# Performance work log

Hardware: AMD Instinct MI355X
Metric: run time of the kernel (lower is better)

## Reference

```python
import jax, jax.numpy as jnp
import numpy as np

B, S, D, H = 2, 2048, 1024, 16
HD = D // H  # head dim 64
LN_EPS = 1e-12


def setup_inputs() -> dict:
    key = jax.random.key(0)
    ks = jax.random.split(key, 10)
    sc = 0.02
    return {
        "input_tensor": jax.random.normal(ks[0], (B, S, D), dtype=jnp.float32),
        "attention_mask": jnp.zeros((B, 1, 1, S), dtype=jnp.float32),
        "Wq": jax.random.normal(ks[1], (D, D), dtype=jnp.float32) * sc,
        "bq": jnp.zeros((D,), dtype=jnp.float32),
        "Wk": jax.random.normal(ks[2], (D, D), dtype=jnp.float32) * sc,
        "bk": jnp.zeros((D,), dtype=jnp.float32),
        "Wv": jax.random.normal(ks[3], (D, D), dtype=jnp.float32) * sc,
        "bv": jnp.zeros((D,), dtype=jnp.float32),
        "Wo": jax.random.normal(ks[4], (D, D), dtype=jnp.float32) * sc,
        "bo": jnp.zeros((D,), dtype=jnp.float32),
        "ln_gamma": jnp.ones((D,), dtype=jnp.float32),
        "ln_beta": jnp.zeros((D,), dtype=jnp.float32),
    }


def _split_heads(x):
    # [B,S,D] -> [B,H,S,hd]
    return x.reshape(B, S, H, HD).transpose(0, 2, 1, 3)


def reference(input_tensor, attention_mask, Wq, bq, Wk, bk, Wv, bv, Wo, bo, ln_gamma, ln_beta):
    q = _split_heads(input_tensor @ Wq + bq)
    k = _split_heads(input_tensor @ Wk + bk)
    v = _split_heads(input_tensor @ Wv + bv)
    scores = jnp.einsum("bhqd,bhkd->bhqk", q, k) / jnp.sqrt(jnp.float32(HD))
    scores = scores + attention_mask  # additive mask broadcast
    probs = jax.nn.softmax(scores, axis=-1)
    ctx = jnp.einsum("bhqk,bhkd->bhqd", probs, v)
    ctx = ctx.transpose(0, 2, 1, 3).reshape(B, S, D)
    hidden = ctx @ Wo + bo
    x = hidden + input_tensor
    mu = jnp.mean(x, axis=-1, keepdims=True)
    var = jnp.mean(jnp.square(x - mu), axis=-1, keepdims=True)
    return (x - mu) / jnp.sqrt(var + LN_EPS) * ln_gamma + ln_beta
```

## Files before the change

### kernel.cpp

```cpp
#include <hip/hip_runtime.h>
#include <stdint.h>

#define Bb 2
#define Ss 2048
#define Dd 1024
#define Hh 16
#define HD 64
#define Mtot 4096

typedef __bf16 bf16x8 __attribute__((ext_vector_type(8)));
typedef float f32x4 __attribute__((ext_vector_type(4)));
typedef unsigned short ushort_t;

#if __has_builtin(__builtin_amdgcn_exp2f)
#define EXP2(x) __builtin_amdgcn_exp2f(x)
#else
#define EXP2(x) __expf((x) * 0.6931472f)
#endif

__device__ __forceinline__ float bf2f(ushort_t u) {
    union { uint32_t i; float f; } v;
    v.i = ((uint32_t)u) << 16;
    return v.f;
}

__device__ __forceinline__ ushort_t f2bf(float f) {
    union { float f; uint32_t i; } v;
    v.f = f;
    uint32_t u = v.i;
    u += 0x7FFFu + ((u >> 16) & 1u);
    return (ushort_t)(u >> 16);
}

__device__ __forceinline__ uint32_t fbits(float f) {
    union { float f; uint32_t i; } v; v.f = f; return v.i;
}

__device__ __forceinline__ float load_in(const void* p, size_t i, int isf32) {
    if (isf32) return ((const float*)p)[i];
    return bf2f(((const ushort_t*)p)[i]);
}

__device__ __forceinline__ void gload_lds16(const void* g, void* l) {
    __builtin_amdgcn_global_load_lds(
        (const __attribute__((address_space(1))) void*)g,
        (__attribute__((address_space(3))) void*)l, 16, 0, 0);
}

#define NCONV 4204544ull
__global__ __launch_bounds__(256) void prep_k(
    const void* X, const void* mask, const void* bq, const void* bk,
    const void* bv, const void* bo, const void* g, const void* be,
    const void* Wq, const void* Wk, const void* Wv, const void* Wo,
    int* __restrict__ flag, ushort_t* __restrict__ cX,
    ushort_t* __restrict__ cMask, ushort_t* __restrict__ cB,
    ushort_t* __restrict__ wt) {
    __shared__ int sflag;
    __shared__ ushort_t tile[32][33];
    const int tid = threadIdx.x;
    {
        const int lane = tid & 63;
        if (tid < 64) {
            const ushort_t* Xu = (const ushort_t*)X;
            int local = 0;
            for (int i = lane; i < 2048; i += 64) {
                int e = (Xu[i] >> 7) & 0xFF;
                local += (e >= 0x90);
            }
            for (int off = 1; off < 64; off <<= 1) local += __shfl_xor(local, off);
            if (lane == 0) sflag = (local >= 4) ? 1 : 0;
        }
    }
    __syncthreads();
    const int f = sflag;
    if (blockIdx.x == 0 && tid == 0) *flag = f;

    if (blockIdx.x < 1024) {
        const size_t stride = 1024ull * 256ull;
        for (size_t i = (size_t)blockIdx.x * 256 + tid; i < NCONV; i += stride) {
            if (i < 4194304ull) {
                cX[i] = f2bf(load_in(X, i, f));
            } else if (i < 4198400ull) {
                size_t j = i - 4194304ull;
                cMask[j] = f2bf(load_in(mask, j, f));
            } else {
                size_t j = i - 4198400ull;
                int w = (int)(j >> 10);
                size_t r = j & 1023ull;
                const void* p = (w == 0) ? bq : (w == 1) ? bk : (w == 2) ? bv
                              : (w == 3) ? bo : (w == 4) ? g : be;
                cB[w * 1024 + r] = f2bf(load_in(p, r, f));
            }
        }
    } else {
        int id2 = blockIdx.x - 1024;
        int z = id2 >> 10;
        int rem = id2 & 1023;
        int bx = rem & 31, by = rem >> 5;
        const void* W = (z == 0) ? Wq : (z == 1) ? Wk : (z == 2) ? Wv : Wo;
        ushort_t* T = wt + (size_t)z * Dd * Dd;
        int tx = tid & 31, ty = tid >> 5;
        int x = bx * 32 + tx;
        int y0 = by * 32;
        for (int i = 0; i < 4; i++) {
            int y = y0 + ty + i * 8;
            tile[ty + i * 8][tx] = f2bf(load_in(W, (size_t)y * Dd + x, f));
        }
        __syncthreads();
        int x2 = by * 32 + tx;
        int y20 = bx * 32;
        for (int i = 0; i < 4; i++) {
            int y = y20 + ty + i * 8;
            T[(size_t)y * Dd + x2] = tile[tx][ty + i * 8];
        }
    }
}

__global__ __launch_bounds__(256) void gemm_qkv(
    const ushort_t* __restrict__ X, const ushort_t* __restrict__ wt,
    const ushort_t* __restrict__ cB,
    ushort_t* __restrict__ Qb, ushort_t* __restrict__ Kb, ushort_t* __restrict__ Vtb) {
    const int z = blockIdx.z;
    const ushort_t* Wt = wt + (size_t)z * Dd * Dd;
    const ushort_t* bias = cB + z * 1024;

    __shared__ __align__(16) ushort_t smem[128 * 32 * 2];
    ushort_t* As = smem;
    ushort_t* Bs = smem + 128 * 32;

    const int tid = threadIdx.x;
    const int lane = tid & 63, wv = tid >> 6;
    const int quad = lane >> 4, l15 = lane & 15;
    const int wrow = (wv >> 1) * 64, wcol = (wv & 1) * 64;
    const int row0 = blockIdx.y * 128, col0 = blockIdx.x * 128;
    const int lrow = lane >> 2, lcol = (lane & 3) * 8;

    const f32x4 fzero = {0.f, 0.f, 0.f, 0.f};
    f32x4 acc[4][4];
    for (int mt = 0; mt < 4; mt++)
        for (int nt = 0; nt < 4; nt++) acc[mt][nt] = fzero;

    for (int k0 = 0; k0 < Dd; k0 += 32) {
        __syncthreads();
        for (int j = 0; j < 2; j++) {
            int ch = wv * 2 + j;
            gload_lds16(&X[(size_t)(row0 + ch * 16 + lrow) * Dd + k0 + lcol],
                        &As[ch * 512]);
            gload_lds16(&Wt[(size_t)(col0 + ch * 16 + lrow) * Dd + k0 + lcol],
                        &Bs[ch * 512]);
        }
        __syncthreads();
        bf16x8 af[4], bfr[4];
        for (int mt = 0; mt < 4; mt++)
            af[mt] = *(const bf16x8*)(&As[(wrow + mt * 16 + l15) * 32 + quad * 8]);
        for (int nt = 0; nt < 4; nt++)
            bfr[nt] = *(const bf16x8*)(&Bs[(wcol + nt * 16 + l15) * 32 + quad * 8]);
        for (int mt = 0; mt < 4; mt++)
            for (int nt = 0; nt < 4; nt++)
                acc[mt][nt] = __builtin_amdgcn_mfma_f32_16x16x32_bf16(
                    af[mt], bfr[nt], acc[mt][nt], 0, 0, 0);
    }

    const float qscale = 0.18033688f;
    ushort_t* Cs = smem;
    for (int mt = 0; mt < 4; mt++) {
        __syncthreads();
        for (int nt = 0; nt < 4; nt++) {
            int gn = col0 + wcol + nt * 16 + l15;
            float bv_ = bf2f(bias[gn]);
            for (int r = 0; r < 4; r++) {
                float v = acc[mt][nt][r] + bv_;
                if (z == 0) v *= qscale;
                int ric = (wv >> 1) * 16 + quad * 4 + r;
                Cs[ric * 136 + wcol + nt * 16 + l15] = f2bf(v);
            }
        }
        __syncthreads();
        if (z == 2) {
            int c = tid >> 1, r0 = (tid & 1) * 16;
            int gn = col0 + c, h = gn >> 6, d = gn & 63;
            int gmbase = row0 + (r0 >> 4) * 64 + mt * 16;
            int b = gmbase >> 11, s0 = gmbase & 2047;
            union { ushort_t u[16]; uint4 q[2]; } pk;
            for (int i = 0; i < 16; i++) pk.u[i] = Cs[(r0 + i) * 136 + c];
            uint4* dst = (uint4*)&Vtb[((size_t)((b * Hh + h) * HD + d)) * Ss + s0];
            dst[0] = pk.q[0];
            dst[1] = pk.q[1];
        } else {
            int ric = tid >> 3, c0 = (tid & 7) * 16;
            int gm = row0 + (ric >> 4) * 64 + mt * 16 + (ric & 15);
            int gn = col0 + c0, h = gn >> 6, d0 = gn & 63;
            int b = gm >> 11, s = gm & 2047;
            const uint4* src = (const uint4*)&Cs[ric * 136 + c0];
            ushort_t* Ob = (z == 0) ? Qb : Kb;
            uint4* dst = (uint4*)&Ob[((size_t)((b * Hh + h) * Ss + s)) * HD + d0];
            dst[0] = src[0];
            dst[1] = src[1];
        }
    }
}

#define STR 76
__global__ __launch_bounds__(512) void attn(
    const ushort_t* __restrict__ Q, const ushort_t* __restrict__ K,
    const ushort_t* __restrict__ Vt, const ushort_t* __restrict__ mask,
    ushort_t* __restrict__ ctx) {
    const int tid = threadIdx.x;
    const int lane = tid & 63, wv = tid >> 6;
    const int quad = lane >> 4, l15 = lane & 15;
    const int bh = blockIdx.x;
    const int b = bh >> 4, h = bh & 15;
    const int q0 = blockIdx.y * 128 + wv * 16;

    const ushort_t* Qh = Q + (size_t)bh * Ss * HD;
    const ushort_t* Kh = K + (size_t)bh * Ss * HD;
    const ushort_t* Vh = Vt + (size_t)bh * HD * Ss;

    __shared__ __align__(16) ushort_t Ks[2][64 * 64];
    __shared__ __align__(16) ushort_t Vs[2][64 * 64];
    __shared__ __align__(16) float maskF[Ss];
    __shared__ __align__(16) ushort_t Pl[8][16 * STR];
    ushort_t* Pw = &Pl[wv][0];

    for (int i = tid; i < Ss; i += 512)
        maskF[i] = (bf2f(mask[b * Ss + i]) - 4.0f) * 1.4426950f;

    const int r8 = lane >> 3, c8 = lane & 7, gc = c8 ^ r8;
    const int sw = l15 & 7;

    gload_lds16(&Kh[(size_t)(wv * 8 + r8) * HD + gc * 8], &Ks[0][wv * 512]);
    gload_lds16(&Vh[(size_t)(wv * 8 + r8) * Ss + gc * 8], &Vs[0][wv * 512]);

    bf16x8 qf[2];
    qf[0] = *(const bf16x8*)(&Qh[(size_t)(q0 + l15) * HD + quad * 8]);
    qf[1] = *(const bf16x8*)(&Qh[(size_t)(q0 + l15) * HD + 32 + quad * 8]);

    const f32x4 fzero = {0.f, 0.f, 0.f, 0.f};
    f32x4 o[4];
    for (int dt = 0; dt < 4; dt++) o[dt] = fzero;
    float l_part = 0.f;

    for (int kb = 0; kb < Ss; kb += 64) {
        const int buf = (kb >> 6) & 1;
        __syncthreads();

        if (kb + 64 < Ss) {
            gload_lds16(&Kh[(size_t)(kb + 64 + wv * 8 + r8) * HD + gc * 8],
                        &Ks[buf ^ 1][wv * 512]);
            gload_lds16(&Vh[(size_t)(wv * 8 + r8) * Ss + kb + 64 + gc * 8],
                        &Vs[buf ^ 1][wv * 512]);
        }

        const ushort_t* ks = &Ks[buf][0];
        const ushort_t* vs = &Vs[buf][0];

        f32x4 st[4];
        for (int kt = 0; kt < 4; kt++) {
            bf16x8 kf0 = *(const bf16x8*)(&ks[(kt * 16 + l15) * 64 + ((quad) ^ sw) * 8]);
            bf16x8 kf1 = *(const bf16x8*)(&ks[(kt * 16 + l15) * 64 + ((quad + 4) ^ sw) * 8]);
            st[kt] = __builtin_amdgcn_mfma_f32_16x16x32_bf16(kf0, qf[0], fzero, 0, 0, 0);
            st[kt] = __builtin_amdgcn_mfma_f32_16x16x32_bf16(kf1, qf[1], st[kt], 0, 0, 0);
        }

        for (int kt = 0; kt < 4; kt++) {
            f32x4 mk = *(const f32x4*)(&maskF[kb + kt * 16 + quad * 4]);
            float e0 = EXP2(st[kt][0] + mk[0]);
            float e1 = EXP2(st[kt][1] + mk[1]);
            float e2 = EXP2(st[kt][2] + mk[2]);
            float e3 = EXP2(st[kt][3] + mk[3]);
            l_part += (e0 + e1) + (e2 + e3);
            uint2 pk;
            pk.x = __builtin_amdgcn_perm(fbits(e1), fbits(e0), 0x07060302u);
            pk.y = __builtin_amdgcn_perm(fbits(e3), fbits(e2), 0x07060302u);
            *(uint2*)(&Pw[l15 * STR + kt * 16 + quad * 4]) = pk;
        }

        for (int c = 0; c < 2; c++) {
            union { uint2 u2[2]; bf16x8 v; } pu;
            pu.u2[0] = *(const uint2*)(&Pw[l15 * STR + c * 32 + quad * 8]);
            pu.u2[1] = *(const uint2*)(&Pw[l15 * STR + c * 32 + quad * 8 + 4]);
            bf16x8 pf = pu.v;
            for (int dt = 0; dt < 4; dt++) {
                bf16x8 vf = *(const bf16x8*)(
                    &vs[(dt * 16 + l15) * 64 + ((c * 4 + quad) ^ sw) * 8]);
                o[dt] = __builtin_amdgcn_mfma_f32_16x16x32_bf16(pf, vf, o[dt], 0, 0, 0);
            }
        }
    }

    float l_q = l_part;
    l_q += __shfl_xor(l_q, 16);
    l_q += __shfl_xor(l_q, 32);

    float linv[4];
    for (int r = 0; r < 4; r++) linv[r] = 1.f / __shfl(l_q, quad * 4 + r);
    for (int r = 0; r < 4; r++) {
        int q = q0 + quad * 4 + r;
        for (int dt = 0; dt < 4; dt++) {
            ctx[((size_t)(b * Ss + q)) * Dd + h * HD + dt * 16 + l15] =
                f2bf(o[dt][r] * linv[r]);
        }
    }
}

__global__ __launch_bounds__(256) void gemm_out(
    const ushort_t* __restrict__ A, const ushort_t* __restrict__ Wt,
    const ushort_t* __restrict__ bo, const ushort_t* __restrict__ X,
    float* __restrict__ xout) {
    __shared__ __align__(16) ushort_t As[64 * 32];
    __shared__ __align__(16) ushort_t Bs[128 * 32];

    const int tid = threadIdx.x;
    const int lane = tid & 63, wv = tid >> 6;
    const int quad = lane >> 4, l15 = lane & 15;
    const int wrow = (wv >> 1) * 32, wcol = (wv & 1) * 64;
    const int row0 = blockIdx.y * 64, col0 = blockIdx.x * 128;
    const int lrow = lane >> 2, lcol = (lane & 3) * 8;

    const f32x4 fzero = {0.f, 0.f, 0.f, 0.f};
    f32x4 acc[2][4];
    for (int mt = 0; mt < 2; mt++)
        for (int nt = 0; nt < 4; nt++) acc[mt][nt] = fzero;

    for (int k0 = 0; k0 < Dd; k0 += 32) {
        __syncthreads();
        gload_lds16(&A[(size_t)(row0 + wv * 16 + lrow) * Dd + k0 + lcol],
                    &As[wv * 512]);
        for (int j = 0; j < 2; j++) {
            int ch = wv * 2 + j;
            gload_lds16(&Wt[(size_t)(col0 + ch * 16 + lrow) * Dd + k0 + lcol],
                        &Bs[ch * 512]);
        }
        __syncthreads();
        bf16x8 af[2], bfr[4];
        for (int mt = 0; mt < 2; mt++)
            af[mt] = *(const bf16x8*)(&As[(wrow + mt * 16 + l15) * 32 + quad * 8]);
        for (int nt = 0; nt < 4; nt++)
            bfr[nt] = *(const bf16x8*)(&Bs[(wcol + nt * 16 + l15) * 32 + quad * 8]);
        for (int mt = 0; mt < 2; mt++)
            for (int nt = 0; nt < 4; nt++)
                acc[mt][nt] = __builtin_amdgcn_mfma_f32_16x16x32_bf16(
                    af[mt], bfr[nt], acc[mt][nt], 0, 0, 0);
    }

    for (int mt = 0; mt < 2; mt++)
        for (int nt = 0; nt < 4; nt++)
            for (int r = 0; r < 4; r++) {
                int gm = row0 + wrow + mt * 16 + quad * 4 + r;
                int gn = col0 + wcol + nt * 16 + l15;
                float v = acc[mt][nt][r] + bf2f(bo[gn]) + bf2f(X[(size_t)gm * Dd + gn]);
                xout[(size_t)gm * Dd + gn] = v;
            }
}

__global__ __launch_bounds__(256) void ln_k(
    const float* __restrict__ x, const ushort_t* __restrict__ gamma,
    const ushort_t* __restrict__ beta, const int* __restrict__ flag,
    void* __restrict__ out) {
    const int row = blockIdx.x;
    const int tid = threadIdx.x;
    const int f = *flag;

    const float4 vv = ((const float4*)(x + (size_t)row * Dd))[tid];
    float s = (vv.x + vv.y) + (vv.z + vv.w);
    float ss = (vv.x * vv.x + vv.y * vv.y) + (vv.z * vv.z + vv.w * vv.w);
    for (int off = 1; off < 64; off <<= 1) {
        s += __shfl_xor(s, off);
        ss += __shfl_xor(ss, off);
    }
    __shared__ float ps[4], pss[4];
    int wv = tid >> 6;
    if ((tid & 63) == 0) { ps[wv] = s; pss[wv] = ss; }
    __syncthreads();
    s = ps[0] + ps[1] + ps[2] + ps[3];
    ss = pss[0] + pss[1] + pss[2] + pss[3];
    float mu = s * (1.f / Dd);
    float var = ss * (1.f / Dd) - mu * mu;
    float rstd = rsqrtf(fmaxf(var, 0.f) + 1e-12f);

    const int c0 = tid * 4;
    float r[4];
    float xi[4] = {vv.x, vv.y, vv.z, vv.w};
    for (int i = 0; i < 4; i++) {
        float g = bf2f(gamma[c0 + i]);
        float bb = bf2f(beta[c0 + i]);
        r[i] = (xi[i] - mu) * rstd * g + bb;
    }
    if (f) {
        float4 o4 = {r[0], r[1], r[2], r[3]};
        ((float4*)out)[(size_t)row * 256 + tid] = o4;
    } else {
        union { ushort_t u[4]; uint2 q; } pk;
        for (int i = 0; i < 4; i++) pk.u[i] = f2bf(r[i]);
        *(uint2*)((ushort_t*)out + (size_t)row * Dd + c0) = pk.q;
    }
}

extern "C" void kernel_launch(void* const* d_in, const int* in_sizes, int n_in,
                              void* d_out, int out_size, void* d_ws, size_t ws_size,
                              hipStream_t stream) {
    char* ws = (char*)d_ws;
    int* flag       = (int*)ws;
    ushort_t* cMask = (ushort_t*)(ws + (64ull << 10));
    ushort_t* cB    = (ushort_t*)(ws + (96ull << 10));
    ushort_t* cX    = (ushort_t*)(ws + (1ull << 20));
    ushort_t* wt    = (ushort_t*)(ws + (17ull << 20));
    ushort_t* Qb    = (ushort_t*)(ws + (25ull << 20));
    ushort_t* Kb    = (ushort_t*)(ws + (33ull << 20));
    ushort_t* Vtb   = (ushort_t*)(ws + (41ull << 20));
    ushort_t* ctx   = (ushort_t*)(ws + (49ull << 20));
    float* xbuf     = (float*)(ws + (25ull << 20));

    hipLaunchKernelGGL(prep_k, dim3(5120), dim3(256), 0, stream,
                       d_in[0], d_in[1], d_in[3], d_in[5], d_in[7], d_in[9],
                       d_in[10], d_in[11], d_in[2], d_in[4], d_in[6], d_in[8],
                       flag, cX, cMask, cB, wt);
    hipLaunchKernelGGL(gemm_qkv, dim3(8, 32, 3), dim3(256), 0, stream,
                       cX, wt, cB, Qb, Kb, Vtb);
    hipLaunchKernelGGL(attn, dim3(32, 16), dim3(512), 0, stream,
                       Qb, Kb, Vtb, cMask, ctx);
    hipLaunchKernelGGL(gemm_out, dim3(8, 64), dim3(256), 0, stream,
                       ctx, wt + 3ull * Dd * Dd, cB + 3 * 1024, cX, xbuf);
    hipLaunchKernelGGL(ln_k, dim3(Mtot), dim3(256), 0, stream,
                       xbuf, cB + 4 * 1024, cB + 5 * 1024, flag, d_out);
}
```

Before: 208.4 us.

## Double-buffer GEMM LDS tiles and fold softmax mask and row-sum into MFMA

The QKV and output-projection GEMMs now prefetch the next K-slice into a second LDS buffer while computing on the current one. This removes one barrier per iteration and overlaps global loads with MFMA work. In attention, the additive mask is used as the initial MFMA accumulator, removing the separate adds. The softmax denominator is now an extra MFMA against a ones vector, replacing the per-lane accumulation and the cross-lane shuffles. The cost is double the LDS use in the GEMMs and one extra MFMA per P chunk; the denominator is now summed from the bf16-rounded probabilities.

```diff
diff --git a/kernel.cpp b/kernel.cpp
--- a/kernel.cpp
+++ b/kernel.cpp
@@ -124,9 +124,7 @@
     const ushort_t* Wt = wt + (size_t)z * Dd * Dd;
     const ushort_t* bias = cB + z * 1024;
 
-    __shared__ __align__(16) ushort_t smem[128 * 32 * 2];
-    ushort_t* As = smem;
-    ushort_t* Bs = smem + 128 * 32;
+    __shared__ __align__(16) ushort_t smem[2][2][128 * 32];
 
     const int tid = threadIdx.x;
     const int lane = tid & 63, wv = tid >> 6;
@@ -140,16 +138,28 @@
     for (int mt = 0; mt < 4; mt++)
         for (int nt = 0; nt < 4; nt++) acc[mt][nt] = fzero;
 
+    for (int j = 0; j < 2; j++) {
+        int ch = wv * 2 + j;
+        gload_lds16(&X[(size_t)(row0 + ch * 16 + lrow) * Dd + lcol],
+                    &smem[0][0][ch * 512]);
+        gload_lds16(&Wt[(size_t)(col0 + ch * 16 + lrow) * Dd + lcol],
+                    &smem[0][1][ch * 512]);
+    }
+
     for (int k0 = 0; k0 < Dd; k0 += 32) {
-        __syncthreads();
-        for (int j = 0; j < 2; j++) {
-            int ch = wv * 2 + j;
-            gload_lds16(&X[(size_t)(row0 + ch * 16 + lrow) * Dd + k0 + lcol],
-                        &As[ch * 512]);
-            gload_lds16(&Wt[(size_t)(col0 + ch * 16 + lrow) * Dd + k0 + lcol],
-                        &Bs[ch * 512]);
-        }
-        __syncthreads();
+        const int buf = (k0 >> 5) & 1;
+        __syncthreads();
+        if (k0 + 32 < Dd) {
+            for (int j = 0; j < 2; j++) {
+                int ch = wv * 2 + j;
+                gload_lds16(&X[(size_t)(row0 + ch * 16 + lrow) * Dd + k0 + 32 + lcol],
+                            &smem[buf ^ 1][0][ch * 512]);
+                gload_lds16(&Wt[(size_t)(col0 + ch * 16 + lrow) * Dd + k0 + 32 + lcol],
+                            &smem[buf ^ 1][1][ch * 512]);
+            }
+        }
+        const ushort_t* As = &smem[buf][0][0];
+        const ushort_t* Bs = &smem[buf][1][0];
         bf16x8 af[4], bfr[4];
         for (int mt = 0; mt < 4; mt++)
             af[mt] = *(const bf16x8*)(&As[(wrow + mt * 16 + l15) * 32 + quad * 8]);
@@ -162,7 +172,7 @@
     }
 
     const float qscale = 0.18033688f;
-    ushort_t* Cs = smem;
+    ushort_t* Cs = &smem[0][0][0];
     for (int mt = 0; mt < 4; mt++) {
         __syncthreads();
         for (int nt = 0; nt < 4; nt++) {
@@ -235,10 +245,17 @@
     qf[0] = *(const bf16x8*)(&Qh[(size_t)(q0 + l15) * HD + quad * 8]);
     qf[1] = *(const bf16x8*)(&Qh[(size_t)(q0 + l15) * HD + 32 + quad * 8]);
 
+    bf16x8 onesf;
+    {
+        union { ushort_t u[8]; bf16x8 v; } ou;
+        for (int i = 0; i < 8; i++) ou.u[i] = 0x3F80;
+        onesf = ou.v;
+    }
+
     const f32x4 fzero = {0.f, 0.f, 0.f, 0.f};
     f32x4 o[4];
     for (int dt = 0; dt < 4; dt++) o[dt] = fzero;
-    float l_part = 0.f;
+    f32x4 o_l = fzero;
 
     for (int kb = 0; kb < Ss; kb += 64) {
         const int buf = (kb >> 6) & 1;
@@ -256,19 +273,18 @@
 
         f32x4 st[4];
         for (int kt = 0; kt < 4; kt++) {
+            f32x4 mk = *(const f32x4*)(&maskF[kb + kt * 16 + quad * 4]);
             bf16x8 kf0 = *(const bf16x8*)(&ks[(kt * 16 + l15) * 64 + ((quad) ^ sw) * 8]);
             bf16x8 kf1 = *(const bf16x8*)(&ks[(kt * 16 + l15) * 64 + ((quad + 4) ^ sw) * 8]);
-            st[kt] = __builtin_amdgcn_mfma_f32_16x16x32_bf16(kf0, qf[0], fzero, 0, 0, 0);
+            st[kt] = __builtin_amdgcn_mfma_f32_16x16x32_bf16(kf0, qf[0], mk, 0, 0, 0);
             st[kt] = __builtin_amdgcn_mfma_f32_16x16x32_bf16(kf1, qf[1], st[kt], 0, 0, 0);
         }
 
         for (int kt = 0; kt < 4; kt++) {
-            f32x4 mk = *(const f32x4*)(&maskF[kb + kt * 16 + quad * 4]);
-            float e0 = EXP2(st[kt][0] + mk[0]);
-            float e1 = EXP2(st[kt][1] + mk[1]);
-            float e2 = EXP2(st[kt][2] + mk[2]);
-            float e3 = EXP2(st[kt][3] + mk[3]);
-            l_part += (e0 + e1) + (e2 + e3);
+            float e0 = EXP2(st[kt][0]);
+            float e1 = EXP2(st[kt][1]);
+            float e2 = EXP2(st[kt][2]);
+            float e3 = EXP2(st[kt][3]);
             uint2 pk;
             pk.x = __builtin_amdgcn_perm(fbits(e1), fbits(e0), 0x07060302u);
             pk.y = __builtin_amdgcn_perm(fbits(e3), fbits(e2), 0x07060302u);
@@ -285,20 +301,16 @@
                     &vs[(dt * 16 + l15) * 64 + ((c * 4 + quad) ^ sw) * 8]);
                 o[dt] = __builtin_amdgcn_mfma_f32_16x16x32_bf16(pf, vf, o[dt], 0, 0, 0);
             }
-        }
-    }
-
-    float l_q = l_part;
-    l_q += __shfl_xor(l_q, 16);
-    l_q += __shfl_xor(l_q, 32);
-
-    float linv[4];
-    for (int r = 0; r < 4; r++) linv[r] = 1.f / __shfl(l_q, quad * 4 + r);
+            o_l = __builtin_amdgcn_mfma_f32_16x16x32_bf16(pf, onesf, o_l, 0, 0, 0);
+        }
+    }
+
     for (int r = 0; r < 4; r++) {
         int q = q0 + quad * 4 + r;
+        float linv = 1.f / o_l[r];
         for (int dt = 0; dt < 4; dt++) {
             ctx[((size_t)(b * Ss + q)) * Dd + h * HD + dt * 16 + l15] =
-                f2bf(o[dt][r] * linv[r]);
+                f2bf(o[dt][r] * linv);
         }
     }
 }
@@ -307,8 +319,7 @@
     const ushort_t* __restrict__ A, const ushort_t* __restrict__ Wt,
     const ushort_t* __restrict__ bo, const ushort_t* __restrict__ X,
     float* __restrict__ xout) {
-    __shared__ __align__(16) ushort_t As[64 * 32];
-    __shared__ __align__(16) ushort_t Bs[128 * 32];
+    __shared__ __align__(16) ushort_t smem[2][6144];
 
     const int tid = threadIdx.x;
     const int lane = tid & 63, wv = tid >> 6;
@@ -322,16 +333,27 @@
     for (int mt = 0; mt < 2; mt++)
         for (int nt = 0; nt < 4; nt++) acc[mt][nt] = fzero;
 
+    gload_lds16(&A[(size_t)(row0 + wv * 16 + lrow) * Dd + lcol], &smem[0][wv * 512]);
+    for (int j = 0; j < 2; j++) {
+        int ch = wv * 2 + j;
+        gload_lds16(&Wt[(size_t)(col0 + ch * 16 + lrow) * Dd + lcol],
+                    &smem[0][2048 + ch * 512]);
+    }
+
     for (int k0 = 0; k0 < Dd; k0 += 32) {
-        __syncthreads();
-        gload_lds16(&A[(size_t)(row0 + wv * 16 + lrow) * Dd + k0 + lcol],
-                    &As[wv * 512]);
-        for (int j = 0; j < 2; j++) {
-            int ch = wv * 2 + j;
-            gload_lds16(&Wt[(size_t)(col0 + ch * 16 + lrow) * Dd + k0 + lcol],
-                        &Bs[ch * 512]);
-        }
-        __syncthreads();
+        const int buf = (k0 >> 5) & 1;
+        __syncthreads();
+        if (k0 + 32 < Dd) {
+            gload_lds16(&A[(size_t)(row0 + wv * 16 + lrow) * Dd + k0 + 32 + lcol],
+                        &smem[buf ^ 1][wv * 512]);
+            for (int j = 0; j < 2; j++) {
+                int ch = wv * 2 + j;
+                gload_lds16(&Wt[(size_t)(col0 + ch * 16 + lrow) * Dd + k0 + 32 + lcol],
+                            &smem[buf ^ 1][2048 + ch * 512]);
+            }
+        }
+        const ushort_t* As = &smem[buf][0];
+        const ushort_t* Bs = &smem[buf][2048];
         bf16x8 af[2], bfr[4];
         for (int mt = 0; mt < 2; mt++)
             af[mt] = *(const bf16x8*)(&As[(wrow + mt * 16 + l15) * 32 + quad * 8]);
```

New measurement: 207.2 us. About the same (-0.5%).
